# Optimization experiments

Measured on AMD Instinct MI355X. Metric: run time of the kernel, lower is better.

## Reference

```python
import jax, jax.numpy as jnp
import numpy as np


def setup_inputs() -> dict:
    key = jax.random.key(0)
    k1, k2, k3 = jax.random.split(key, 3)
    B, S, D = 128, 1024, 64
    return {
        "q": jax.random.normal(k1, (B, S, D), dtype=jnp.float32),
        "k": jax.random.normal(k2, (B, S, D), dtype=jnp.float32),
        "v": jax.random.normal(k3, (B, S, D), dtype=jnp.float32),
    }


def reference(q, k, v):
    # Faithful to the torch module: NO 1/sqrt(d) scaling.
    # Chunking over batch dim in the original is math-equivalent to full bmm.
    scores = jnp.einsum("bsd,btd->bst", q, k)  # [B, S, S]
    attn = jax.nn.softmax(scores, axis=-1)
    return jnp.einsum("bst,btd->bsd", attn, v)  # [B, S, D]
```

## Files before the change

kernel.cpp:

```cpp
#include <hip/hip_runtime.h>
#include <math.h>

namespace {

typedef _Float16 half8 __attribute__((ext_vector_type(8)));
typedef float floatx4 __attribute__((ext_vector_type(4)));

constexpr int kS   = 1024;
constexpr int kD   = 64;
constexpr int kPad = 72;
constexpr float kLog2e = 1.4426950408889634f;

union H4 { _Float16 h[4]; uint2 u2; };

__device__ __forceinline__ float fast_exp2(float x) {
#if __has_builtin(__builtin_amdgcn_exp2f)
  return __builtin_amdgcn_exp2f(x);
#else
  return exp2f(x);
#endif
}

__device__ __forceinline__ float fast_rcp(float x) {
#if __has_builtin(__builtin_amdgcn_rcpf)
  return __builtin_amdgcn_rcpf(x);
#else
  return 1.0f / x;
#endif
}

__global__ __launch_bounds__(256, 3)
void fa_mfma_kernel(const float* __restrict__ qg, const float* __restrict__ kg,
                    const float* __restrict__ vg, float* __restrict__ og) {
  __shared__ __align__(16) _Float16 sK [64][kPad];
  __shared__ __align__(16) _Float16 sVt[64][kPad];
  __shared__ __align__(16) _Float16 sP [128][kPad];

  const int tid  = threadIdx.x;
  const int lane = tid & 63;
  const int w    = __builtin_amdgcn_readfirstlane(tid >> 6);
  const int quad = lane >> 4;
  const int r    = lane & 15;

  const int blk = blockIdx.x;
  const int s   = blk >> 3;
  const int b   = (blk & 7) + 8 * (s & 15);
  const int qbase = (s >> 4) * 128;

  const float* qb = qg + (size_t)b * kS * kD;
  const float* kb = kg + (size_t)b * kS * kD;
  const float* vb = vg + (size_t)b * kS * kD;
  float*       ob = og + (size_t)b * kS * kD;

  half8 fqh[2][2], fql[2][2];
#pragma unroll
  for (int ntq = 0; ntq < 2; ++ntq)
#pragma unroll
    for (int ks = 0; ks < 2; ++ks) {
      const float* src =
          qb + (size_t)(qbase + w * 32 + ntq * 16 + r) * kD + ks * 32 + quad * 8;
      float4 a = ((const float4*)src)[0];
      float4 c = ((const float4*)src)[1];
      float f[8] = {a.x, a.y, a.z, a.w, c.x, c.y, c.z, c.w};
#pragma unroll
      for (int j = 0; j < 8; ++j) {
        float x = f[j] * kLog2e;
        _Float16 h = (_Float16)x;
        fqh[ntq][ks][j] = h;
        fql[ntq][ks][j] = (_Float16)(x - (float)h);
      }
    }

  float m_i[2] = {-INFINITY, -INFINITY}, l_i[2] = {0.f, 0.f};
  floatx4 O[2][4];
#pragma unroll
  for (int a = 0; a < 2; ++a)
#pragma unroll
    for (int c = 0; c < 4; ++c) O[a][c] = floatx4{0.f, 0.f, 0.f, 0.f};

  const int krow = tid >> 2, kc0 = (tid & 3) * 16;
  const int vkey = tid & 63, vd0 = (tid >> 6) * 16;
  float4 kbuf[4], vbuf[4];
  {
    const float4* ksrc = (const float4*)(kb + (size_t)krow * kD + kc0);
    const float4* vsrc = (const float4*)(vb + (size_t)vkey * kD + vd0);
#pragma unroll
    for (int g = 0; g < 4; ++g) { kbuf[g] = ksrc[g]; vbuf[g] = vsrc[g]; }
  }

  for (int kt = 0; kt < kS / 64; ++kt) {
    __syncthreads();
#pragma unroll
    for (int g = 0; g < 4; ++g) {
      float t[4] = {kbuf[g].x, kbuf[g].y, kbuf[g].z, kbuf[g].w};
      H4 hk;
#pragma unroll
      for (int j = 0; j < 4; ++j) hk.h[j] = (_Float16)t[j];
      *(uint2*)&sK[krow][kc0 + g * 4] = hk.u2;
    }
#pragma unroll
    for (int g = 0; g < 4; ++g) {
      float t[4] = {vbuf[g].x, vbuf[g].y, vbuf[g].z, vbuf[g].w};
#pragma unroll
      for (int j = 0; j < 4; ++j) sVt[vd0 + g * 4 + j][vkey] = (_Float16)t[j];
    }
    {
      const int ktn = (kt + 1) & 15;
      const float4* ksrc =
          (const float4*)(kb + (size_t)(ktn * 64 + krow) * kD + kc0);
      const float4* vsrc =
          (const float4*)(vb + (size_t)(ktn * 64 + vkey) * kD + vd0);
#pragma unroll
      for (int g = 0; g < 4; ++g) { kbuf[g] = ksrc[g]; vbuf[g] = vsrc[g]; }
    }
    __syncthreads();

    floatx4 S[2][4];
#pragma unroll
    for (int mt = 0; mt < 4; ++mt) {
      half8 fk0 = *(const half8*)&sK[mt * 16 + r][0 * 32 + quad * 8];
      half8 fk1 = *(const half8*)&sK[mt * 16 + r][1 * 32 + quad * 8];
#pragma unroll
      for (int ntq = 0; ntq < 2; ++ntq) {
        floatx4 ah = {0.f, 0.f, 0.f, 0.f}, al = {0.f, 0.f, 0.f, 0.f};
        ah = __builtin_amdgcn_mfma_f32_16x16x32_f16(fk0, fqh[ntq][0], ah, 0, 0, 0);
        ah = __builtin_amdgcn_mfma_f32_16x16x32_f16(fk1, fqh[ntq][1], ah, 0, 0, 0);
        al = __builtin_amdgcn_mfma_f32_16x16x32_f16(fk0, fql[ntq][0], al, 0, 0, 0);
        al = __builtin_amdgcn_mfma_f32_16x16x32_f16(fk1, fql[ntq][1], al, 0, 0, 0);
        S[ntq][mt] = ah + al;
      }
    }

    float alpha[2];
#pragma unroll
    for (int ntq = 0; ntq < 2; ++ntq) {
      float tm = -INFINITY;
#pragma unroll
      for (int mt = 0; mt < 4; ++mt)
#pragma unroll
        for (int j = 0; j < 4; ++j) tm = fmaxf(tm, S[ntq][mt][j]);
      tm = fmaxf(tm, __shfl_xor(tm, 16, 64));
      tm = fmaxf(tm, __shfl_xor(tm, 32, 64));
      const float mn = fmaxf(m_i[ntq], tm);
      alpha[ntq] = fast_exp2(m_i[ntq] - mn);
      float rs = 0.f;
#pragma unroll
      for (int mt = 0; mt < 4; ++mt) {
        H4 hp;
#pragma unroll
        for (int j = 0; j < 4; ++j) {
          float pj = fast_exp2(S[ntq][mt][j] - mn);
          rs += pj;
          hp.h[j] = (_Float16)pj;
        }
        *(uint2*)&sP[w * 32 + ntq * 16 + r][mt * 16 + quad * 4] = hp.u2;
      }
      rs += __shfl_xor(rs, 16, 64);
      rs += __shfl_xor(rs, 32, 64);
      l_i[ntq] = l_i[ntq] * alpha[ntq] + rs;
      m_i[ntq] = mn;
    }

#pragma unroll
    for (int mtq = 0; mtq < 2; ++mtq)
#pragma unroll
      for (int j = 0; j < 4; ++j) {
        const float a = __shfl(alpha[mtq], quad * 4 + j, 64);
#pragma unroll
        for (int nd = 0; nd < 4; ++nd) O[mtq][nd][j] *= a;
      }

#pragma unroll
    for (int ks = 0; ks < 2; ++ks) {
      half8 fp0 = *(const half8*)&sP[w * 32 + 0 * 16 + r][ks * 32 + quad * 8];
      half8 fp1 = *(const half8*)&sP[w * 32 + 1 * 16 + r][ks * 32 + quad * 8];
#pragma unroll
      for (int nd = 0; nd < 4; ++nd) {
        half8 fv = *(const half8*)&sVt[nd * 16 + r][ks * 32 + quad * 8];
        O[0][nd] = __builtin_amdgcn_mfma_f32_16x16x32_f16(fp0, fv, O[0][nd], 0, 0, 0);
        O[1][nd] = __builtin_amdgcn_mfma_f32_16x16x32_f16(fp1, fv, O[1][nd], 0, 0, 0);
      }
    }
  }

#pragma unroll
  for (int mtq = 0; mtq < 2; ++mtq)
#pragma unroll
    for (int j = 0; j < 4; ++j) {
      const float lrow = __shfl(l_i[mtq], quad * 4 + j, 64);
      const float linv = fast_rcp(lrow);
      float* dst =
          ob + (size_t)(qbase + w * 32 + mtq * 16 + quad * 4 + j) * kD + r;
#pragma unroll
      for (int nd = 0; nd < 4; ++nd) dst[nd * 16] = O[mtq][nd][j] * linv;
    }
}

}

extern "C" void kernel_launch(void* const* d_in, const int* in_sizes, int n_in,
                              void* d_out, int out_size, void* d_ws, size_t ws_size,
                              hipStream_t stream) {
  const float* q = (const float*)d_in[0];
  const float* k = (const float*)d_in[1];
  const float* v = (const float*)d_in[2];
  float* out = (float*)d_out;

  fa_mfma_kernel<<<dim3(1024), 256, 0, stream>>>(q, k, v, out);
}
```

Measured before the change: 203.4 us.

## Add lazy softmax rescaling, vectorized V transpose stores, setprio and occupancy 4

Skips the running-max update and the O/l rescale unless some row's tile max exceeds the stored max by more than a threshold, decided wave-uniformly through a ballot. Restructures the V load so each thread loads four keys and writes packed 4-half values into the transposed shared tile instead of scalar half stores. Wraps the MFMA sections in s_setprio and raises launch bounds to 4 blocks per CU. The lazy rescale lets exp2 arguments reach up to 2^8 in fp16 P, which risks precision loss or overflow near the fp16 limit.

After: 304.4 us. 1.5x slower.

```diff
diff --git a/kernel.cpp b/kernel.cpp
--- a/kernel.cpp
+++ b/kernel.cpp
@@ -10,6 +10,7 @@
 constexpr int kD   = 64;
 constexpr int kPad = 72;
 constexpr float kLog2e = 1.4426950408889634f;
+constexpr float kThr   = 8.0f;
 
 union H4 { _Float16 h[4]; uint2 u2; };
 
@@ -29,7 +30,7 @@
 #endif
 }
 
-__global__ __launch_bounds__(256, 3)
+__global__ __launch_bounds__(256, 4)
 void fa_mfma_kernel(const float* __restrict__ qg, const float* __restrict__ kg,
                     const float* __restrict__ vg, float* __restrict__ og) {
   __shared__ __align__(16) _Float16 sK [64][kPad];
@@ -79,13 +80,16 @@
     for (int c = 0; c < 4; ++c) O[a][c] = floatx4{0.f, 0.f, 0.f, 0.f};
 
   const int krow = tid >> 2, kc0 = (tid & 3) * 16;
-  const int vkey = tid & 63, vd0 = (tid >> 6) * 16;
+  const int vkey4 = (tid & 15) * 4;
+  const int vd0   = (tid >> 4) * 4;
   float4 kbuf[4], vbuf[4];
   {
     const float4* ksrc = (const float4*)(kb + (size_t)krow * kD + kc0);
-    const float4* vsrc = (const float4*)(vb + (size_t)vkey * kD + vd0);
-#pragma unroll
-    for (int g = 0; g < 4; ++g) { kbuf[g] = ksrc[g]; vbuf[g] = vsrc[g]; }
+#pragma unroll
+    for (int g = 0; g < 4; ++g) kbuf[g] = ksrc[g];
+#pragma unroll
+    for (int kk = 0; kk < 4; ++kk)
+      vbuf[kk] = *(const float4*)(vb + (size_t)(vkey4 + kk) * kD + vd0);
   }
 
   for (int kt = 0; kt < kS / 64; ++kt) {
@@ -98,24 +102,36 @@
       for (int j = 0; j < 4; ++j) hk.h[j] = (_Float16)t[j];
       *(uint2*)&sK[krow][kc0 + g * 4] = hk.u2;
     }
-#pragma unroll
-    for (int g = 0; g < 4; ++g) {
-      float t[4] = {vbuf[g].x, vbuf[g].y, vbuf[g].z, vbuf[g].w};
-#pragma unroll
-      for (int j = 0; j < 4; ++j) sVt[vd0 + g * 4 + j][vkey] = (_Float16)t[j];
+    {
+      float tv[4][4];
+#pragma unroll
+      for (int kk = 0; kk < 4; ++kk) {
+        tv[kk][0] = vbuf[kk].x; tv[kk][1] = vbuf[kk].y;
+        tv[kk][2] = vbuf[kk].z; tv[kk][3] = vbuf[kk].w;
+      }
+#pragma unroll
+      for (int j = 0; j < 4; ++j) {
+        H4 hv;
+#pragma unroll
+        for (int kk = 0; kk < 4; ++kk) hv.h[kk] = (_Float16)tv[kk][j];
+        *(uint2*)&sVt[vd0 + j][vkey4] = hv.u2;
+      }
     }
     {
       const int ktn = (kt + 1) & 15;
       const float4* ksrc =
           (const float4*)(kb + (size_t)(ktn * 64 + krow) * kD + kc0);
-      const float4* vsrc =
-          (const float4*)(vb + (size_t)(ktn * 64 + vkey) * kD + vd0);
-#pragma unroll
-      for (int g = 0; g < 4; ++g) { kbuf[g] = ksrc[g]; vbuf[g] = vsrc[g]; }
+#pragma unroll
+      for (int g = 0; g < 4; ++g) kbuf[g] = ksrc[g];
+#pragma unroll
+      for (int kk = 0; kk < 4; ++kk)
+        vbuf[kk] =
+            *(const float4*)(vb + (size_t)(ktn * 64 + vkey4 + kk) * kD + vd0);
     }
     __syncthreads();
 
     floatx4 S[2][4];
+    __builtin_amdgcn_s_setprio(1);
 #pragma unroll
     for (int mt = 0; mt < 4; ++mt) {
       half8 fk0 = *(const half8*)&sK[mt * 16 + r][0 * 32 + quad * 8];
@@ -130,26 +146,49 @@
         S[ntq][mt] = ah + al;
       }
     }
-
-    float alpha[2];
+    __builtin_amdgcn_s_setprio(0);
+
+    float tm[2];
 #pragma unroll
     for (int ntq = 0; ntq < 2; ++ntq) {
-      float tm = -INFINITY;
+      float t = -INFINITY;
 #pragma unroll
       for (int mt = 0; mt < 4; ++mt)
 #pragma unroll
-        for (int j = 0; j < 4; ++j) tm = fmaxf(tm, S[ntq][mt][j]);
-      tm = fmaxf(tm, __shfl_xor(tm, 16, 64));
-      tm = fmaxf(tm, __shfl_xor(tm, 32, 64));
-      const float mn = fmaxf(m_i[ntq], tm);
-      alpha[ntq] = fast_exp2(m_i[ntq] - mn);
+        for (int j = 0; j < 4; ++j) t = fmaxf(t, S[ntq][mt][j]);
+      t = fmaxf(t, __shfl_xor(t, 16, 64));
+      t = fmaxf(t, __shfl_xor(t, 32, 64));
+      tm[ntq] = t;
+    }
+    const unsigned long long need =
+        __ballot(tm[0] > m_i[0] + kThr || tm[1] > m_i[1] + kThr);
+    if (need) {
+      float alpha[2];
+#pragma unroll
+      for (int ntq = 0; ntq < 2; ++ntq) {
+        const float mn = fmaxf(m_i[ntq], tm[ntq]);
+        alpha[ntq] = fast_exp2(m_i[ntq] - mn);
+        m_i[ntq] = mn;
+        l_i[ntq] *= alpha[ntq];
+      }
+#pragma unroll
+      for (int mtq = 0; mtq < 2; ++mtq)
+#pragma unroll
+        for (int j = 0; j < 4; ++j) {
+          const float a = __shfl(alpha[mtq], quad * 4 + j, 64);
+#pragma unroll
+          for (int nd = 0; nd < 4; ++nd) O[mtq][nd][j] *= a;
+        }
+    }
+#pragma unroll
+    for (int ntq = 0; ntq < 2; ++ntq) {
       float rs = 0.f;
 #pragma unroll
       for (int mt = 0; mt < 4; ++mt) {
         H4 hp;
 #pragma unroll
         for (int j = 0; j < 4; ++j) {
-          float pj = fast_exp2(S[ntq][mt][j] - mn);
+          float pj = fast_exp2(S[ntq][mt][j] - m_i[ntq]);
           rs += pj;
           hp.h[j] = (_Float16)pj;
         }
@@ -157,19 +196,10 @@
       }
       rs += __shfl_xor(rs, 16, 64);
       rs += __shfl_xor(rs, 32, 64);
-      l_i[ntq] = l_i[ntq] * alpha[ntq] + rs;
-      m_i[ntq] = mn;
-    }
-
-#pragma unroll
-    for (int mtq = 0; mtq < 2; ++mtq)
-#pragma unroll
-      for (int j = 0; j < 4; ++j) {
-        const float a = __shfl(alpha[mtq], quad * 4 + j, 64);
-#pragma unroll
-        for (int nd = 0; nd < 4; ++nd) O[mtq][nd][j] *= a;
-      }
-
+      l_i[ntq] += rs;
+    }
+
+    __builtin_amdgcn_s_setprio(1);
 #pragma unroll
     for (int ks = 0; ks < 2; ++ks) {
       half8 fp0 = *(const half8*)&sP[w * 32 + 0 * 16 + r][ks * 32 + quad * 8];
@@ -181,6 +211,7 @@
         O[1][nd] = __builtin_amdgcn_mfma_f32_16x16x32_f16(fp1, fv, O[1][nd], 0, 0, 0);
       }
     }
+    __builtin_amdgcn_s_setprio(0);
   }
 
 #pragma unroll
```
